# Kernel optimization log

Hardware: AMD Instinct MI355X
Metric: run time of the kernel (lower is better)

## Reference

```python
import jax, jax.numpy as jnp
import numpy as np

N_NODES = 50000


def _sage_layer(x, src, tgt, W, b):
    # mean aggregation of neighbor (source) features at target nodes
    msgs = x[src]  # [E, d] gather
    summed = jax.ops.segment_sum(msgs, tgt, num_segments=N_NODES)
    deg = jax.ops.segment_sum(jnp.ones((src.shape[0],), x.dtype), tgt,
                              num_segments=N_NODES)
    aggr = summed / jnp.maximum(deg, 1.0)[:, None]
    concat = jnp.concatenate([x, aggr], axis=1)  # [N, 2d]
    return jax.nn.relu(concat @ W + b)


def setup_inputs() -> dict:
    key = jax.random.key(0)
    k1, k2, k3, k4 = jax.random.split(key, 4)
    x = jax.random.normal(k1, (N_NODES, 128), dtype=jnp.float32)
    edge_index = jax.random.randint(k2, (2, 800000), 0, N_NODES, dtype=jnp.int64)
    # Linear(in=2*d, out=hidden); store as [in, out] for x @ W + b
    s1 = 1.0 / np.sqrt(256.0)
    W1 = jax.random.uniform(k3, (256, 128), jnp.float32, -s1, s1)
    b1 = jnp.zeros((128,), jnp.float32)
    W2 = jax.random.uniform(k4, (256, 128), jnp.float32, -s1, s1)
    b2 = jnp.zeros((128,), jnp.float32)
    return {"x": x, "edge_index": edge_index, "W1": W1, "b1": b1,
            "W2": W2, "b2": b2}


def reference(x, edge_index, W1, b1, W2, b2):
    src, tgt = edge_index[0], edge_index[1]
    h = _sage_layer(x, src, tgt, W1, b1)
    # F.relu on already-relu'd output is identity; dropout inactive in eval
    out = _sage_layer(h, src, tgt, W2, b2)
    return out
```

## Files before the change

### kernel.cpp

```cpp
#include <hip/hip_runtime.h>

#define D 128
#define NPB 128
#define BSH 7
typedef unsigned int uint;
typedef unsigned short ushort;
typedef __attribute__((ext_vector_type(8))) __bf16 bf16x8;
typedef __attribute__((ext_vector_type(4))) float f32x4;

__device__ __forceinline__ ushort f2bf(float f) {
    uint u = __float_as_uint(f);
    u += 0x7fffu + ((u >> 16) & 1u);
    return (ushort)(u >> 16);
}


__global__ __launch_bounds__(256) void bhist_k(const int* __restrict__ tgt,
                                               int* __restrict__ bhist,
                                               int E, int NBKT) {
    __shared__ int lh[512];
    for (int t = threadIdx.x; t < NBKT; t += 256) lh[t] = 0;
    __syncthreads();
    int i0 = blockIdx.x * 4096 + threadIdx.x * 4;
#pragma unroll
    for (int k = 0; k < 4; ++k) {
        int i = i0 + k * 1024;
        if (i + 3 < E) {
            int4 v = *reinterpret_cast<const int4*>(tgt + i);
            atomicAdd(&lh[v.x >> BSH], 1);
            atomicAdd(&lh[v.y >> BSH], 1);
            atomicAdd(&lh[v.z >> BSH], 1);
            atomicAdd(&lh[v.w >> BSH], 1);
        } else {
            for (int j = 0; j < 4; ++j)
                if (i + j < E) atomicAdd(&lh[tgt[i + j] >> BSH], 1);
        }
    }
    __syncthreads();
    for (int t = threadIdx.x; t < NBKT; t += 256)
        if (lh[t]) atomicAdd(&bhist[t], lh[t]);
}


__global__ __launch_bounds__(512) void bscan_k(const int* __restrict__ bhist,
                                               int* __restrict__ bbase,
                                               int* __restrict__ bcur,
                                               int* __restrict__ row_ptr,
                                               int NBKT, int N) {
    int t = threadIdx.x;
    int v = (t < NBKT) ? bhist[t] : 0;
    int lane = t & 63, w = t >> 6;
    int inc = v;
#pragma unroll
    for (int off = 1; off < 64; off <<= 1) {
        int u = __shfl_up(inc, off);
        if (lane >= off) inc += u;
    }
    __shared__ int wt[8];
    if (lane == 63) wt[w] = inc;
    __syncthreads();
    int add = 0;
    for (int i = 0; i < w; ++i) add += wt[i];
    int excl = inc - v + add;
    if (t < NBKT) { bbase[t] = excl; bcur[t] = excl; }
    if (t == NBKT - 1) row_ptr[N] = excl + v;
}


__global__ __launch_bounds__(256) void passA_k(const int* __restrict__ src,
                                               const int* __restrict__ tgt,
                                               int* __restrict__ bcur,
                                               int* __restrict__ staging,
                                               int E, int NBKT) {
    __shared__ int lh[512], lb[512];
    for (int t = threadIdx.x; t < NBKT; t += 256) lh[t] = 0;
    __syncthreads();
    int i0 = blockIdx.x * 4096 + threadIdx.x * 4;
    int sv[16], tv[16], rk[16];
#pragma unroll
    for (int k = 0; k < 4; ++k) {
        int i = i0 + k * 1024;
        if (i + 3 < E) {
            int4 s4 = *reinterpret_cast<const int4*>(src + i);
            int4 t4 = *reinterpret_cast<const int4*>(tgt + i);
            sv[k * 4 + 0] = s4.x; tv[k * 4 + 0] = t4.x;
            sv[k * 4 + 1] = s4.y; tv[k * 4 + 1] = t4.y;
            sv[k * 4 + 2] = s4.z; tv[k * 4 + 2] = t4.z;
            sv[k * 4 + 3] = s4.w; tv[k * 4 + 3] = t4.w;
        } else {
            for (int j = 0; j < 4; ++j) {
                if (i + j < E) { sv[k * 4 + j] = src[i + j]; tv[k * 4 + j] = tgt[i + j]; }
                else tv[k * 4 + j] = -1;
            }
        }
#pragma unroll
        for (int j = 0; j < 4; ++j) {
            int e = k * 4 + j;
            rk[e] = (tv[e] >= 0) ? atomicAdd(&lh[tv[e] >> BSH], 1) : 0;
        }
    }
    __syncthreads();
    for (int t = threadIdx.x; t < NBKT; t += 256)
        lb[t] = lh[t] ? atomicAdd(&bcur[t], lh[t]) : 0;
    __syncthreads();
#pragma unroll
    for (int e = 0; e < 16; ++e) {
        if (tv[e] >= 0) {
            int b = tv[e] >> BSH;
            staging[lb[b] + rk[e]] = (sv[e] << BSH) | (tv[e] & (NPB - 1));
        }
    }
}


__global__ __launch_bounds__(256) void passB_k(const int* __restrict__ bbase,
                                               const int* __restrict__ staging,
                                               int* __restrict__ row_ptr,
                                               int* __restrict__ srcs,
                                               int N, int NBKT, int E) {
    int b = blockIdx.x;
    int s = bbase[b];
    int e = (b + 1 < NBKT) ? bbase[b + 1] : E;
    int t = threadIdx.x;
    __shared__ int nh[NPB], nb[NPB];
    __shared__ int w0tot;
    if (t < NPB) nh[t] = 0;
    __syncthreads();
    for (int i = s + t; i < e; i += 256)
        atomicAdd(&nh[staging[i] & (NPB - 1)], 1);
    __syncthreads();
    int v = 0, inc = 0;
    if (t < NPB) {
        v = nh[t];
        inc = v;
        int lane = t & 63;
#pragma unroll
        for (int off = 1; off < 64; off <<= 1) {
            int u = __shfl_up(inc, off);
            if (lane >= off) inc += u;
        }
        if (lane == 63 && t < 64) w0tot = inc;
    }
    __syncthreads();
    if (t < NPB) {
        int excl = inc - v + ((t >= 64) ? w0tot : 0);
        nb[t] = s + excl;
        int node = b * NPB + t;
        if (node < N) row_ptr[node] = s + excl;
        nh[t] = 0;
    }
    __syncthreads();
    for (int i = s + t; i < e; i += 256) {
        int pv = staging[i];
        int tl = pv & (NPB - 1);
        int p = nb[tl] + atomicAdd(&nh[tl], 1);
        srcs[p] = pv >> BSH;
    }
}


__global__ __launch_bounds__(256) void prep_k(
    const float* __restrict__ x, ushort* __restrict__ xb, int n8, int CB,
    const float* __restrict__ W1, ushort* __restrict__ wp1,
    const float* __restrict__ W2, ushort* __restrict__ wp2) {
    int b = blockIdx.x;
    if (b < CB) {
        int i = b * 256 + threadIdx.x;
        if (i < n8) {
            const float4* s = reinterpret_cast<const float4*>(x) + (size_t)i * 2;
            float4 a = s[0], c = s[1];
            ushort4 o0, o1;
            o0.x = f2bf(a.x); o0.y = f2bf(a.y); o0.z = f2bf(a.z); o0.w = f2bf(a.w);
            o1.x = f2bf(c.x); o1.y = f2bf(c.y); o1.z = f2bf(c.z); o1.w = f2bf(c.w);
            reinterpret_cast<ushort4*>(xb)[(size_t)i * 2] = o0;
            reinterpret_cast<ushort4*>(xb)[(size_t)i * 2 + 1] = o1;
        }
    } else {
        int pb = b - CB;
        const float* __restrict__ W = (pb < 16) ? W1 : W2;
        ushort* __restrict__ wp = (pb < 16) ? wp1 : wp2;
        int idx = (pb & 15) * 256 + threadIdx.x;
        int lane = idx & 63;
        int ct = (idx >> 6) & 7;
        int ks = idx >> 9;
        int col = ct * 16 + (lane & 15);
        int k0 = ks * 32 + (lane >> 4) * 8;
        ushort v[8];
#pragma unroll
        for (int e = 0; e < 8; ++e) v[e] = f2bf(W[(size_t)(k0 + e) * D + col]);
        ushort4 lo4; lo4.x = v[0]; lo4.y = v[1]; lo4.z = v[2]; lo4.w = v[3];
        ushort4 hi4; hi4.x = v[4]; hi4.y = v[5]; hi4.z = v[6]; hi4.w = v[7];
        reinterpret_cast<ushort4*>(wp + (size_t)idx * 8)[0] = lo4;
        reinterpret_cast<ushort4*>(wp + (size_t)idx * 8)[1] = hi4;
    }
}


__global__ __launch_bounds__(256) void aggr_k(const ushort* __restrict__ Xb,
                                              const int* __restrict__ srcs,
                                              const int* __restrict__ row_ptr,
                                              ushort* __restrict__ aggr, int N) {
    int node = blockIdx.x * 4 + (threadIdx.x >> 6);
    if (node >= N) return;
    int lane = threadIdx.x & 63;
    int g = lane >> 4, l = lane & 15;
    int lo = row_ptr[node], hi = row_ptr[node + 1];
    float acc[8] = {0.f, 0.f, 0.f, 0.f, 0.f, 0.f, 0.f, 0.f};
    for (int base = lo; base < hi; base += 64) {
        int idx = base + lane;
        int sv = (idx < hi) ? srcs[idx] : -1;
        int cnt = min(64, hi - base);
        for (int e = 0; e < cnt; e += 16) {
            int ss[4];
#pragma unroll
            for (int q = 0; q < 4; ++q) ss[q] = __shfl(sv, e + q * 4 + g);
            uint4 vv[4];
#pragma unroll
            for (int q = 0; q < 4; ++q) {
                vv[q].x = 0; vv[q].y = 0; vv[q].z = 0; vv[q].w = 0;
            }
#pragma unroll
            for (int q = 0; q < 4; ++q)
                if (ss[q] >= 0)
                    vv[q] = *reinterpret_cast<const uint4*>(Xb + (size_t)ss[q] * D + l * 8);
#pragma unroll
            for (int q = 0; q < 4; ++q) {
                acc[0] += __uint_as_float(vv[q].x << 16);
                acc[1] += __uint_as_float(vv[q].x & 0xffff0000u);
                acc[2] += __uint_as_float(vv[q].y << 16);
                acc[3] += __uint_as_float(vv[q].y & 0xffff0000u);
                acc[4] += __uint_as_float(vv[q].z << 16);
                acc[5] += __uint_as_float(vv[q].z & 0xffff0000u);
                acc[6] += __uint_as_float(vv[q].w << 16);
                acc[7] += __uint_as_float(vv[q].w & 0xffff0000u);
            }
        }
    }
#pragma unroll
    for (int j = 0; j < 8; ++j) {
        acc[j] += __shfl_xor(acc[j], 16);
        acc[j] += __shfl_xor(acc[j], 32);
    }
    if (g == 0) {
        float inv = 1.0f / fmaxf((float)(hi - lo), 1.0f);
        ushort4 o0, o1;
        o0.x = f2bf(acc[0] * inv); o0.y = f2bf(acc[1] * inv);
        o0.z = f2bf(acc[2] * inv); o0.w = f2bf(acc[3] * inv);
        o1.x = f2bf(acc[4] * inv); o1.y = f2bf(acc[5] * inv);
        o1.z = f2bf(acc[6] * inv); o1.w = f2bf(acc[7] * inv);
        ushort* dst = aggr + (size_t)node * D + l * 8;
        reinterpret_cast<ushort4*>(dst)[0] = o0;
        reinterpret_cast<ushort4*>(dst)[1] = o1;
    }
}


__global__ __launch_bounds__(256) void gemm_k(
    const ushort* __restrict__ Xb, const ushort* __restrict__ Ab,
    const ushort* __restrict__ Wp, const float* __restrict__ bias,
    float* __restrict__ outf, ushort* __restrict__ outb, int n) {
    int lane = threadIdx.x & 63;
    int w = threadIdx.x >> 6;
    int row_base = blockIdx.x * 64 + (w & 1) * 32;
    int ct0 = (w >> 1) * 4;
    int r0 = row_base + (lane & 15);
    int r1 = row_base + 16 + (lane & 15);
    if (r0 > n - 1) r0 = n - 1;
    if (r1 > n - 1) r1 = n - 1;
    int klo = (lane >> 4) * 8;

    f32x4 acc[2][4] = {};
#pragma unroll
    for (int ks = 0; ks < 8; ++ks) {
        const ushort* __restrict__ S = (ks < 4) ? Xb : Ab;
        int koff = (ks & 3) * 32 + klo;
        bf16x8 a0 = *reinterpret_cast<const bf16x8*>(S + (size_t)r0 * D + koff);
        bf16x8 a1 = *reinterpret_cast<const bf16x8*>(S + (size_t)r1 * D + koff);
        const ushort* wb = Wp + ((size_t)(ks * 8 + ct0) * 64 + lane) * 8;
#pragma unroll
        for (int c = 0; c < 4; ++c) {
            bf16x8 b = *reinterpret_cast<const bf16x8*>(wb + (size_t)c * 64 * 8);
            acc[0][c] = __builtin_amdgcn_mfma_f32_16x16x32_bf16(a0, b, acc[0][c], 0, 0, 0);
            acc[1][c] = __builtin_amdgcn_mfma_f32_16x16x32_bf16(a1, b, acc[1][c], 0, 0, 0);
        }
    }

    int cw = lane & 15;
    int rq = lane >> 4;
#pragma unroll
    for (int rt = 0; rt < 2; ++rt) {
#pragma unroll
        for (int c = 0; c < 4; ++c) {
            int col = (ct0 + c) * 16 + cw;
            float bv = bias[col];
#pragma unroll
            for (int r = 0; r < 4; ++r) {
                int node = row_base + rt * 16 + rq * 4 + r;
                if (node < n) {
                    float v = fmaxf(acc[rt][c][r] + bv, 0.f);
                    if (outf) outf[(size_t)node * D + col] = v;
                    if (outb) outb[(size_t)node * D + col] = f2bf(v);
                }
            }
        }
    }
}

extern "C" void kernel_launch(void* const* d_in, const int* in_sizes, int n_in,
                              void* d_out, int out_size, void* d_ws, size_t ws_size,
                              hipStream_t stream) {
    const float* x  = (const float*)d_in[0];
    const int*   ei = (const int*)d_in[1];
    const float* W1 = (const float*)d_in[2];
    const float* b1 = (const float*)d_in[3];
    const float* W2 = (const float*)d_in[4];
    const float* b2 = (const float*)d_in[5];
    float* out = (float*)d_out;

    const int N = in_sizes[0] / D;
    const int E = in_sizes[1] / 2;
    const int* src = ei;
    const int* tgt = ei + E;

    char* w = (char*)d_ws;
    auto alloc = [&](size_t bytes) -> char* {
        char* p = w;
        w += ((bytes + 255) / 256) * 256;
        return p;
    };
    const int NBKT = (N + NPB - 1) / NPB;
    int*    row_ptr = (int*)alloc((size_t)(N + 1) * 4);
    int*    bhist   = (int*)alloc((size_t)NBKT * 4);
    int*    bbase   = (int*)alloc((size_t)NBKT * 4);
    int*    bcur    = (int*)alloc((size_t)NBKT * 4);
    int*    staging = (int*)alloc((size_t)E * 4);
    int*    srcs    = (int*)alloc((size_t)E * 4);
    ushort* xb      = (ushort*)alloc((size_t)N * D * 2);
    ushort* h1b     = (ushort*)alloc((size_t)N * D * 2);
    ushort* ab      = (ushort*)alloc((size_t)N * D * 2);
    ushort* wp1     = (ushort*)alloc((size_t)8 * 8 * 64 * 8 * 2);
    ushort* wp2     = (ushort*)alloc((size_t)8 * 8 * 64 * 8 * 2);

    const int EB = (E + 4095) / 4096;
    const int n8 = N * D / 8;
    const int CB = (n8 + 255) / 256;

    hipMemsetAsync(bhist, 0, (size_t)NBKT * sizeof(int), stream);
    bhist_k<<<EB, 256, 0, stream>>>(tgt, bhist, E, NBKT);
    prep_k<<<CB + 32, 256, 0, stream>>>(x, xb, n8, CB, W1, wp1, W2, wp2);
    bscan_k<<<1, 512, 0, stream>>>(bhist, bbase, bcur, row_ptr, NBKT, N);
    passA_k<<<EB, 256, 0, stream>>>(src, tgt, bcur, staging, E, NBKT);
    passB_k<<<NBKT, 256, 0, stream>>>(bbase, staging, row_ptr, srcs, N, NBKT, E);

    aggr_k<<<(N + 3) / 4, 256, 0, stream>>>(xb, srcs, row_ptr, ab, N);
    gemm_k<<<(N + 63) / 64, 256, 0, stream>>>(xb, ab, wp1, b1, nullptr, h1b, N);

    aggr_k<<<(N + 3) / 4, 256, 0, stream>>>(h1b, srcs, row_ptr, ab, N);
    gemm_k<<<(N + 63) / 64, 256, 0, stream>>>(h1b, ab, wp2, b2, out, nullptr, N);
}
```

Before: 207.6 us.

## Fuse mean aggregation with GEMM via LDS tile and merge histogram into prep

Measured after the change: 211.1 us. No clear change (+1.7%).

```diff
diff --git a/kernel.cpp b/kernel.cpp
--- a/kernel.cpp
+++ b/kernel.cpp
@@ -15,30 +15,63 @@
 }
 
 
-__global__ __launch_bounds__(256) void bhist_k(const int* __restrict__ tgt,
-                                               int* __restrict__ bhist,
-                                               int E, int NBKT) {
+__global__ __launch_bounds__(256) void prep_k(
+    const int* __restrict__ tgt, int* __restrict__ bhist, int E, int HB,
+    const float* __restrict__ x, ushort* __restrict__ xb, int n8, int CB,
+    const float* __restrict__ W1, ushort* __restrict__ wp1,
+    const float* __restrict__ W2, ushort* __restrict__ wp2, int NBKT) {
     __shared__ int lh[512];
-    for (int t = threadIdx.x; t < NBKT; t += 256) lh[t] = 0;
-    __syncthreads();
-    int i0 = blockIdx.x * 4096 + threadIdx.x * 4;
-#pragma unroll
-    for (int k = 0; k < 4; ++k) {
-        int i = i0 + k * 1024;
-        if (i + 3 < E) {
-            int4 v = *reinterpret_cast<const int4*>(tgt + i);
-            atomicAdd(&lh[v.x >> BSH], 1);
-            atomicAdd(&lh[v.y >> BSH], 1);
-            atomicAdd(&lh[v.z >> BSH], 1);
-            atomicAdd(&lh[v.w >> BSH], 1);
-        } else {
-            for (int j = 0; j < 4; ++j)
-                if (i + j < E) atomicAdd(&lh[tgt[i + j] >> BSH], 1);
-        }
-    }
-    __syncthreads();
-    for (int t = threadIdx.x; t < NBKT; t += 256)
-        if (lh[t]) atomicAdd(&bhist[t], lh[t]);
+    int b = blockIdx.x;
+    if (b < HB) {
+        for (int t = threadIdx.x; t < NBKT; t += 256) lh[t] = 0;
+        __syncthreads();
+        int i0 = b * 4096 + threadIdx.x * 4;
+#pragma unroll
+        for (int k = 0; k < 4; ++k) {
+            int i = i0 + k * 1024;
+            if (i + 3 < E) {
+                int4 v = *reinterpret_cast<const int4*>(tgt + i);
+                atomicAdd(&lh[v.x >> BSH], 1);
+                atomicAdd(&lh[v.y >> BSH], 1);
+                atomicAdd(&lh[v.z >> BSH], 1);
+                atomicAdd(&lh[v.w >> BSH], 1);
+            } else {
+                for (int j = 0; j < 4; ++j)
+                    if (i + j < E) atomicAdd(&lh[tgt[i + j] >> BSH], 1);
+            }
+        }
+        __syncthreads();
+        for (int t = threadIdx.x; t < NBKT; t += 256)
+            if (lh[t]) atomicAdd(&bhist[t], lh[t]);
+    } else if (b < HB + CB) {
+        int i = (b - HB) * 256 + threadIdx.x;
+        if (i < n8) {
+            const float4* s = reinterpret_cast<const float4*>(x) + (size_t)i * 2;
+            float4 a = s[0], c = s[1];
+            ushort4 o0, o1;
+            o0.x = f2bf(a.x); o0.y = f2bf(a.y); o0.z = f2bf(a.z); o0.w = f2bf(a.w);
+            o1.x = f2bf(c.x); o1.y = f2bf(c.y); o1.z = f2bf(c.z); o1.w = f2bf(c.w);
+            reinterpret_cast<ushort4*>(xb)[(size_t)i * 2] = o0;
+            reinterpret_cast<ushort4*>(xb)[(size_t)i * 2 + 1] = o1;
+        }
+    } else {
+        int pb = b - HB - CB;
+        const float* __restrict__ W = (pb < 16) ? W1 : W2;
+        ushort* __restrict__ wp = (pb < 16) ? wp1 : wp2;
+        int idx = (pb & 15) * 256 + threadIdx.x;
+        int lane = idx & 63;
+        int ct = (idx >> 6) & 7;
+        int ks = idx >> 9;
+        int col = ct * 16 + (lane & 15);
+        int k0 = ks * 32 + (lane >> 4) * 8;
+        ushort v[8];
+#pragma unroll
+        for (int e = 0; e < 8; ++e) v[e] = f2bf(W[(size_t)(k0 + e) * D + col]);
+        ushort4 lo4; lo4.x = v[0]; lo4.y = v[1]; lo4.z = v[2]; lo4.w = v[3];
+        ushort4 hi4; hi4.x = v[4]; hi4.y = v[5]; hi4.z = v[6]; hi4.w = v[7];
+        reinterpret_cast<ushort4*>(wp + (size_t)idx * 8)[0] = lo4;
+        reinterpret_cast<ushort4*>(wp + (size_t)idx * 8)[1] = hi4;
+    }
 }
 
 
@@ -159,148 +192,111 @@
 }
 
 
-__global__ __launch_bounds__(256) void prep_k(
-    const float* __restrict__ x, ushort* __restrict__ xb, int n8, int CB,
-    const float* __restrict__ W1, ushort* __restrict__ wp1,
-    const float* __restrict__ W2, ushort* __restrict__ wp2) {
-    int b = blockIdx.x;
-    if (b < CB) {
-        int i = b * 256 + threadIdx.x;
-        if (i < n8) {
-            const float4* s = reinterpret_cast<const float4*>(x) + (size_t)i * 2;
-            float4 a = s[0], c = s[1];
+__global__ __launch_bounds__(256) void fused_k(
+    const ushort* __restrict__ Xb, const int* __restrict__ srcs,
+    const int* __restrict__ row_ptr, const ushort* __restrict__ Wp,
+    const float* __restrict__ bias, float* __restrict__ outf,
+    ushort* __restrict__ outb, int n) {
+    __shared__ ushort lab[32][D];
+    int tid = threadIdx.x;
+    int w = tid >> 6;
+    int lane = tid & 63;
+    int g = lane >> 4, l = lane & 15;
+    int node_base = blockIdx.x * 32;
+
+    for (int i = 0; i < 8; ++i) {
+        int node = node_base + w * 8 + i;
+        int lo = 0, hi = 0;
+        if (node < n) { lo = row_ptr[node]; hi = row_ptr[node + 1]; }
+        float acc[8] = {0.f, 0.f, 0.f, 0.f, 0.f, 0.f, 0.f, 0.f};
+        for (int base = lo; base < hi; base += 64) {
+            int idx = base + lane;
+            int sv = (idx < hi) ? srcs[idx] : -1;
+            int cnt = min(64, hi - base);
+            for (int e = 0; e < cnt; e += 16) {
+                int ss[4];
+#pragma unroll
+                for (int q = 0; q < 4; ++q) ss[q] = __shfl(sv, e + q * 4 + g);
+                uint4 vv[4];
+#pragma unroll
+                for (int q = 0; q < 4; ++q) {
+                    vv[q].x = 0; vv[q].y = 0; vv[q].z = 0; vv[q].w = 0;
+                }
+#pragma unroll
+                for (int q = 0; q < 4; ++q)
+                    if (ss[q] >= 0)
+                        vv[q] = *reinterpret_cast<const uint4*>(Xb + (size_t)ss[q] * D + l * 8);
+#pragma unroll
+                for (int q = 0; q < 4; ++q) {
+                    acc[0] += __uint_as_float(vv[q].x << 16);
+                    acc[1] += __uint_as_float(vv[q].x & 0xffff0000u);
+                    acc[2] += __uint_as_float(vv[q].y << 16);
+                    acc[3] += __uint_as_float(vv[q].y & 0xffff0000u);
+                    acc[4] += __uint_as_float(vv[q].z << 16);
+                    acc[5] += __uint_as_float(vv[q].z & 0xffff0000u);
+                    acc[6] += __uint_as_float(vv[q].w << 16);
+                    acc[7] += __uint_as_float(vv[q].w & 0xffff0000u);
+                }
+            }
+        }
+#pragma unroll
+        for (int j = 0; j < 8; ++j) {
+            acc[j] += __shfl_xor(acc[j], 16);
+            acc[j] += __shfl_xor(acc[j], 32);
+        }
+        if (g == 0) {
+            float inv = 1.0f / fmaxf((float)(hi - lo), 1.0f);
+            int r = w * 8 + i;
+            ushort* dst = &lab[r][(l ^ (r & 15)) * 8];
             ushort4 o0, o1;
-            o0.x = f2bf(a.x); o0.y = f2bf(a.y); o0.z = f2bf(a.z); o0.w = f2bf(a.w);
-            o1.x = f2bf(c.x); o1.y = f2bf(c.y); o1.z = f2bf(c.z); o1.w = f2bf(c.w);
-            reinterpret_cast<ushort4*>(xb)[(size_t)i * 2] = o0;
-            reinterpret_cast<ushort4*>(xb)[(size_t)i * 2 + 1] = o1;
-        }
-    } else {
-        int pb = b - CB;
-        const float* __restrict__ W = (pb < 16) ? W1 : W2;
-        ushort* __restrict__ wp = (pb < 16) ? wp1 : wp2;
-        int idx = (pb & 15) * 256 + threadIdx.x;
-        int lane = idx & 63;
-        int ct = (idx >> 6) & 7;
-        int ks = idx >> 9;
-        int col = ct * 16 + (lane & 15);
-        int k0 = ks * 32 + (lane >> 4) * 8;
-        ushort v[8];
-#pragma unroll
-        for (int e = 0; e < 8; ++e) v[e] = f2bf(W[(size_t)(k0 + e) * D + col]);
-        ushort4 lo4; lo4.x = v[0]; lo4.y = v[1]; lo4.z = v[2]; lo4.w = v[3];
-        ushort4 hi4; hi4.x = v[4]; hi4.y = v[5]; hi4.z = v[6]; hi4.w = v[7];
-        reinterpret_cast<ushort4*>(wp + (size_t)idx * 8)[0] = lo4;
-        reinterpret_cast<ushort4*>(wp + (size_t)idx * 8)[1] = hi4;
-    }
-}
-
-
-__global__ __launch_bounds__(256) void aggr_k(const ushort* __restrict__ Xb,
-                                              const int* __restrict__ srcs,
-                                              const int* __restrict__ row_ptr,
-                                              ushort* __restrict__ aggr, int N) {
-    int node = blockIdx.x * 4 + (threadIdx.x >> 6);
-    if (node >= N) return;
-    int lane = threadIdx.x & 63;
-    int g = lane >> 4, l = lane & 15;
-    int lo = row_ptr[node], hi = row_ptr[node + 1];
-    float acc[8] = {0.f, 0.f, 0.f, 0.f, 0.f, 0.f, 0.f, 0.f};
-    for (int base = lo; base < hi; base += 64) {
-        int idx = base + lane;
-        int sv = (idx < hi) ? srcs[idx] : -1;
-        int cnt = min(64, hi - base);
-        for (int e = 0; e < cnt; e += 16) {
-            int ss[4];
-#pragma unroll
-            for (int q = 0; q < 4; ++q) ss[q] = __shfl(sv, e + q * 4 + g);
-            uint4 vv[4];
-#pragma unroll
-            for (int q = 0; q < 4; ++q) {
-                vv[q].x = 0; vv[q].y = 0; vv[q].z = 0; vv[q].w = 0;
-            }
-#pragma unroll
-            for (int q = 0; q < 4; ++q)
-                if (ss[q] >= 0)
-                    vv[q] = *reinterpret_cast<const uint4*>(Xb + (size_t)ss[q] * D + l * 8);
-#pragma unroll
-            for (int q = 0; q < 4; ++q) {
-                acc[0] += __uint_as_float(vv[q].x << 16);
-                acc[1] += __uint_as_float(vv[q].x & 0xffff0000u);
-                acc[2] += __uint_as_float(vv[q].y << 16);
-                acc[3] += __uint_as_float(vv[q].y & 0xffff0000u);
-                acc[4] += __uint_as_float(vv[q].z << 16);
-                acc[5] += __uint_as_float(vv[q].z & 0xffff0000u);
-                acc[6] += __uint_as_float(vv[q].w << 16);
-                acc[7] += __uint_as_float(vv[q].w & 0xffff0000u);
-            }
-        }
-    }
-#pragma unroll
-    for (int j = 0; j < 8; ++j) {
-        acc[j] += __shfl_xor(acc[j], 16);
-        acc[j] += __shfl_xor(acc[j], 32);
-    }
-    if (g == 0) {
-        float inv = 1.0f / fmaxf((float)(hi - lo), 1.0f);
-        ushort4 o0, o1;
-        o0.x = f2bf(acc[0] * inv); o0.y = f2bf(acc[1] * inv);
-        o0.z = f2bf(acc[2] * inv); o0.w = f2bf(acc[3] * inv);
-        o1.x = f2bf(acc[4] * inv); o1.y = f2bf(acc[5] * inv);
-        o1.z = f2bf(acc[6] * inv); o1.w = f2bf(acc[7] * inv);
-        ushort* dst = aggr + (size_t)node * D + l * 8;
-        reinterpret_cast<ushort4*>(dst)[0] = o0;
-        reinterpret_cast<ushort4*>(dst)[1] = o1;
-    }
-}
-
-
-__global__ __launch_bounds__(256) void gemm_k(
-    const ushort* __restrict__ Xb, const ushort* __restrict__ Ab,
-    const ushort* __restrict__ Wp, const float* __restrict__ bias,
-    float* __restrict__ outf, ushort* __restrict__ outb, int n) {
-    int lane = threadIdx.x & 63;
-    int w = threadIdx.x >> 6;
-    int row_base = blockIdx.x * 64 + (w & 1) * 32;
+            o0.x = f2bf(acc[0] * inv); o0.y = f2bf(acc[1] * inv);
+            o0.z = f2bf(acc[2] * inv); o0.w = f2bf(acc[3] * inv);
+            o1.x = f2bf(acc[4] * inv); o1.y = f2bf(acc[5] * inv);
+            o1.z = f2bf(acc[6] * inv); o1.w = f2bf(acc[7] * inv);
+            *reinterpret_cast<ushort4*>(dst) = o0;
+            *reinterpret_cast<ushort4*>(dst + 4) = o1;
+        }
+    }
+    __syncthreads();
+
+    int rbl = (w & 1) * 16;
+    int row_base = node_base + rbl;
     int ct0 = (w >> 1) * 4;
-    int r0 = row_base + (lane & 15);
-    int r1 = row_base + 16 + (lane & 15);
+    int r0 = row_base + l;
     if (r0 > n - 1) r0 = n - 1;
-    if (r1 > n - 1) r1 = n - 1;
-    int klo = (lane >> 4) * 8;
-
-    f32x4 acc[2][4] = {};
+    int klo = g * 8;
+
+    f32x4 acc2[4] = {};
 #pragma unroll
     for (int ks = 0; ks < 8; ++ks) {
-        const ushort* __restrict__ S = (ks < 4) ? Xb : Ab;
-        int koff = (ks & 3) * 32 + klo;
-        bf16x8 a0 = *reinterpret_cast<const bf16x8*>(S + (size_t)r0 * D + koff);
-        bf16x8 a1 = *reinterpret_cast<const bf16x8*>(S + (size_t)r1 * D + koff);
+        bf16x8 a0;
+        if (ks < 4) {
+            int koff = ks * 32 + klo;
+            a0 = *reinterpret_cast<const bf16x8*>(Xb + (size_t)r0 * D + koff);
+        } else {
+            int ch = (ks & 3) * 4 + g;
+            int rl = rbl + l;
+            a0 = *reinterpret_cast<const bf16x8*>(&lab[rl][(ch ^ l) * 8]);
+        }
         const ushort* wb = Wp + ((size_t)(ks * 8 + ct0) * 64 + lane) * 8;
 #pragma unroll
         for (int c = 0; c < 4; ++c) {
             bf16x8 b = *reinterpret_cast<const bf16x8*>(wb + (size_t)c * 64 * 8);
-            acc[0][c] = __builtin_amdgcn_mfma_f32_16x16x32_bf16(a0, b, acc[0][c], 0, 0, 0);
-            acc[1][c] = __builtin_amdgcn_mfma_f32_16x16x32_bf16(a1, b, acc[1][c], 0, 0, 0);
-        }
-    }
-
-    int cw = lane & 15;
-    int rq = lane >> 4;
-#pragma unroll
-    for (int rt = 0; rt < 2; ++rt) {
-#pragma unroll
-        for (int c = 0; c < 4; ++c) {
-            int col = (ct0 + c) * 16 + cw;
-            float bv = bias[col];
-#pragma unroll
-            for (int r = 0; r < 4; ++r) {
-                int node = row_base + rt * 16 + rq * 4 + r;
-                if (node < n) {
-                    float v = fmaxf(acc[rt][c][r] + bv, 0.f);
-                    if (outf) outf[(size_t)node * D + col] = v;
-                    if (outb) outb[(size_t)node * D + col] = f2bf(v);
-                }
+            acc2[c] = __builtin_amdgcn_mfma_f32_16x16x32_bf16(a0, b, acc2[c], 0, 0, 0);
+        }
+    }
+
+#pragma unroll
+    for (int c = 0; c < 4; ++c) {
+        int col = (ct0 + c) * 16 + l;
+        float bv = bias[col];
+#pragma unroll
+        for (int r = 0; r < 4; ++r) {
+            int node = node_base + rbl + g * 4 + r;
+            if (node < n) {
+                float v = fmaxf(acc2[c][r] + bv, 0.f);
+                if (outf) outf[(size_t)node * D + col] = v;
+                if (outb) outb[(size_t)node * D + col] = f2bf(v);
             }
         }
     }
@@ -337,7 +333,6 @@
     int*    srcs    = (int*)alloc((size_t)E * 4);
     ushort* xb      = (ushort*)alloc((size_t)N * D * 2);
     ushort* h1b     = (ushort*)alloc((size_t)N * D * 2);
-    ushort* ab      = (ushort*)alloc((size_t)N * D * 2);
     ushort* wp1     = (ushort*)alloc((size_t)8 * 8 * 64 * 8 * 2);
     ushort* wp2     = (ushort*)alloc((size_t)8 * 8 * 64 * 8 * 2);
 
@@ -346,15 +341,15 @@
     const int CB = (n8 + 255) / 256;
 
     hipMemsetAsync(bhist, 0, (size_t)NBKT * sizeof(int), stream);
-    bhist_k<<<EB, 256, 0, stream>>>(tgt, bhist, E, NBKT);
-    prep_k<<<CB + 32, 256, 0, stream>>>(x, xb, n8, CB, W1, wp1, W2, wp2);
+    prep_k<<<EB + CB + 32, 256, 0, stream>>>(tgt, bhist, E, EB,
+                                             x, xb, n8, CB,
+                                             W1, wp1, W2, wp2, NBKT);
     bscan_k<<<1, 512, 0, stream>>>(bhist, bbase, bcur, row_ptr, NBKT, N);
     passA_k<<<EB, 256, 0, stream>>>(src, tgt, bcur, staging, E, NBKT);
     passB_k<<<NBKT, 256, 0, stream>>>(bbase, staging, row_ptr, srcs, N, NBKT, E);
 
-    aggr_k<<<(N + 3) / 4, 256, 0, stream>>>(xb, srcs, row_ptr, ab, N);
-    gemm_k<<<(N + 63) / 64, 256, 0, stream>>>(xb, ab, wp1, b1, nullptr, h1b, N);
-
-    aggr_k<<<(N + 3) / 4, 256, 0, stream>>>(h1b, srcs, row_ptr, ab, N);
-    gemm_k<<<(N + 63) / 64, 256, 0, stream>>>(h1b, ab, wp2, b2, out, nullptr, N);
-}
+    fused_k<<<(N + 31) / 32, 256, 0, stream>>>(xb, srcs, row_ptr, wp1, b1,
+                                               nullptr, h1b, N);
+    fused_k<<<(N + 31) / 32, 256, 0, stream>>>(h1b, srcs, row_ptr, wp2, b2,
+                                               out, nullptr, N);
+}
```
